# Performance work log

Measured on AMD Instinct MI355X. Metric: run time of the kernel, lower is better.

The kernel has to match this reference:

```python
import jax, jax.numpy as jnp
import numpy as np
import math

D_MODEL = 1024
EXPAND = 2
D_INNER = D_MODEL * EXPAND          # 2048
D_STATE = 16
NHEADS = 8
NGROUPS = 1
D_CONV = 4
HEADDIM = D_INNER // NHEADS         # 256
CONV_DIM = D_INNER + 2 * NGROUPS * D_STATE   # x, B, C go through the causal conv
D_IN_PROJ = 2 * D_INNER + 2 * NGROUPS * D_STATE + NHEADS  # z, xBC, dt
CHUNK = 64
BATCH = 4
SEQLEN = 4096


def setup_inputs() -> dict:
    key = jax.random.key(0)
    ks = jax.random.split(key, 6)
    rng = np.random.default_rng(0)
    u = jax.random.normal(ks[0], (BATCH, SEQLEN, D_MODEL), dtype=jnp.float32)
    W_in = jax.random.normal(ks[1], (D_MODEL, D_IN_PROJ), dtype=jnp.float32) * 0.02
    conv_w = jax.random.normal(ks[2], (CONV_DIM, D_CONV), dtype=jnp.float32) * (1.0 / math.sqrt(D_CONV))
    conv_b = jnp.zeros((CONV_DIM,), dtype=jnp.float32)
    # dt_bias = inverse-softplus of dt sampled log-uniform in [dt_min, dt_max]
    dt = np.exp(rng.uniform(size=NHEADS) * (math.log(0.1) - math.log(0.001)) + math.log(0.001))
    dt = np.clip(dt, 1e-4, None)
    dt_bias = jnp.asarray(dt + np.log(-np.expm1(-dt)), dtype=jnp.float32)
    # A in A_init_range=(0.9, 0.999), stored as A_log with A = -exp(A_log)
    A_log = jnp.asarray(np.log(rng.uniform(0.9, 0.999, NHEADS)), dtype=jnp.float32)
    D = jnp.ones((NHEADS,), dtype=jnp.float32)
    norm_w = jnp.ones((D_INNER,), dtype=jnp.float32)
    W_out = jax.random.normal(ks[3], (D_INNER, D_MODEL), dtype=jnp.float32) * 0.02
    return {"u": u, "W_in": W_in, "conv_w": conv_w, "conv_b": conv_b,
            "dt_bias": dt_bias, "A_log": A_log, "D": D, "norm_w": norm_w, "W_out": W_out}


def _mamba2_fwd(u, W_in, conv_w, conv_b, dt_bias, A_log, D, norm_w, W_out):
    b, l, _ = u.shape
    h, p, n, g, Q = NHEADS, HEADDIM, D_STATE, NGROUPS, CHUNK
    zxbcdt = u @ W_in                                   # [b,l,2*d_inner+2gn+h]
    z = zxbcdt[..., :D_INNER]
    xBC = zxbcdt[..., D_INNER:D_INNER + CONV_DIM]
    dt = jax.nn.softplus(zxbcdt[..., D_INNER + CONV_DIM:] + dt_bias)  # [b,l,h]
    # causal depthwise conv over time (d_conv taps) + SiLU
    xp = jnp.pad(xBC, ((0, 0), (D_CONV - 1, 0), (0, 0)))
    xconv = conv_b
    for k in range(D_CONV):
        xconv = xconv + xp[:, k:k + l, :] * conv_w[:, k]
    xBC = jax.nn.silu(xconv)
    x = xBC[..., :D_INNER].reshape(b, l, h, p)
    B = xBC[..., D_INNER:D_INNER + g * n].reshape(b, l, g, n)
    C = xBC[..., D_INNER + g * n:].reshape(b, l, g, n)
    Bh = jnp.repeat(B, h // g, axis=2)                  # [b,l,h,n]
    Ch = jnp.repeat(C, h // g, axis=2)
    A = -jnp.exp(A_log)                                 # [h]
    # ---- chunked (SSD) selective scan ----
    nc = l // Q
    xc = x.reshape(b, nc, Q, h, p)
    dtc = dt.reshape(b, nc, Q, h)
    Bc = Bh.reshape(b, nc, Q, h, n)
    Cc = Ch.reshape(b, nc, Q, h, n)
    a = dtc * A                                         # [b,nc,Q,h]
    cs = jnp.cumsum(a, axis=2).transpose(0, 1, 3, 2)    # [b,nc,h,Q]
    mask = jnp.tril(jnp.ones((Q, Q), dtype=bool))
    L = jnp.where(mask, jnp.exp(cs[..., :, None] - cs[..., None, :]), 0.0)  # [b,nc,h,Q,Q]
    xdt = xc * dtc[..., None]                           # x scaled by dt
    Y_diag = jnp.einsum('bcqhn,bcshn,bchqs,bcshp->bcqhp', Cc, Bc, L, xdt)
    decay_states = jnp.exp(cs[..., -1:] - cs)           # [b,nc,h,Q]
    states = jnp.einsum('bcqhn,bchq,bcqhp->bchpn', Bc, decay_states, xdt)  # per-chunk state
    chunk_decay = jnp.exp(cs[..., -1])                  # [b,nc,h]
    def step(carry, inp):
        st, dec = inp
        new = dec[..., None, None] * carry + st
        return new, carry
    init = jnp.zeros((b, h, p, n), dtype=u.dtype)
    _, prev = jax.lax.scan(step, init, (states.transpose(1, 0, 2, 3, 4), chunk_decay.transpose(1, 0, 2)))
    prev = prev.transpose(1, 0, 2, 3, 4)                # state entering each chunk [b,nc,h,p,n]
    Y_off = jnp.einsum('bcqhn,bchpn,bchq->bcqhp', Cc, prev, jnp.exp(cs))
    y = (Y_diag + Y_off).reshape(b, l, h, p) + D[:, None] * x
    y = y.reshape(b, l, D_INNER)
    # gated RMSNorm then out projection
    y = y * jax.nn.silu(z)
    y = y * jax.lax.rsqrt(jnp.mean(y * y, axis=-1, keepdims=True) + 1e-5) * norm_w
    return y @ W_out


def reference(u, W_in, conv_w, conv_b, dt_bias, A_log, D, norm_w, W_out):
    return _mamba2_fwd(u, W_in, conv_w, conv_b, dt_bias, A_log, D, norm_w, W_out)
```

## Files before the change

### kernel.cpp

```cpp
#include <hip/hip_runtime.h>
#include <cstddef>
#include <cstdint>

constexpr int DM = 1024;
constexpr int DI = 2048;
constexpr int DS = 16;
constexpr int NH = 8;
constexpr int CD = 2080;
constexpr int DP = 4136;
constexpr int DPT = 4352;
constexpr int Q  = 64;
constexpr int B_ = 4;
constexpr int L_ = 4096;
constexpr int NCH = 64;
constexpr int HP = 256;
constexpr int NR = B_ * L_;

constexpr size_t AL(size_t x) { return (x + 255) & ~(size_t)255; }
constexpr size_t OFFB_ZX = 0;
constexpr size_t OFFB_BC = AL(OFFB_ZX + (size_t)NR * DP * 2);
constexpr size_t OFFB_DT = AL(OFFB_BC + (size_t)NR * 32 * 4);
constexpr size_t OFFB_CS = AL(OFFB_DT + (size_t)NR * NH * 4);
constexpr size_t OFFB_ST = AL(OFFB_CS + (size_t)B_ * NCH * NH * Q * 4);
constexpr size_t OFFB_Y  = AL(OFFB_ST + (size_t)B_ * NCH * NH * HP * DS * 4);
constexpr size_t OFFB_WO = AL(OFFB_Y + (size_t)NR * DI * 2);

__device__ __forceinline__ float silu_f(float x) { return x / (1.f + expf(-x)); }
__device__ __forceinline__ float bf2f(unsigned short v) {
  unsigned int u = ((unsigned int)v) << 16;
  return __builtin_bit_cast(float, u);
}
__device__ __forceinline__ unsigned short f2bf(float f) {
  unsigned int u = __builtin_bit_cast(unsigned int, f);
  u += 0x7FFFu + ((u >> 16) & 1u);
  return (unsigned short)(u >> 16);
}

typedef __attribute__((ext_vector_type(8))) short bf16x8;
typedef __attribute__((ext_vector_type(4))) float f32x4;

__device__ __forceinline__ void bar() {
  asm volatile("" ::: "memory");
  __builtin_amdgcn_s_barrier();
  asm volatile("" ::: "memory");
}

template<bool OUT_BF16>
__global__ __launch_bounds__(512, 2)
void gemm256(const unsigned short* __restrict__ A, const unsigned short* __restrict__ Bt,
             void* __restrict__ Cout, int M, int N, int K, int ldc) {
  __shared__ __align__(16) unsigned short lds[2][2][2][256 * 32];
  const int t = threadIdx.x;
  const int w = t >> 6, l = t & 63;
  const int quad = l >> 4, lan = l & 15;
  const int wm = w >> 2, wn = w & 3;
  const int ncol = gridDim.x;
  const int id = blockIdx.y * ncol + blockIdx.x;
  const int xcd = id & 7, slot0 = id >> 3;
  const int rpx = gridDim.y >> 3;
  const int row_g = xcd * rpx + slot0 / ncol;
  const int col_g = slot0 - (slot0 / ncol) * ncol;
  const int row0 = row_g * 256, col0 = col_g * 256;

  const int NT = K >> 6;

  auto stage = [&](int tt, int kk, int mat) {
    const int ss = (tt < NT) ? tt : 0;
    const unsigned short* G = mat ? Bt : A;
    const int b0 = mat ? col0 : row0;
    unsigned short* lb = lds[tt & 1][kk][mat];
    const int k0 = (ss << 6) + (kk << 5);
    #pragma unroll
    for (int i = 0; i < 2; ++i) {
      const int f = i * 512 + t;
      const int pair = f >> 3, sp = f & 7;
      const int sl = sp ^ (pair & 7);
      const int r = pair * 2 + (sl >> 2);
      const int c16 = sl & 3;
      const unsigned short* gp = G + (size_t)(b0 + r) * K + k0 + (c16 << 3);
      __builtin_amdgcn_global_load_lds(
          (const __attribute__((address_space(1))) void*)gp,
          (__attribute__((address_space(3))) void*)(lb + (size_t)f * 8), 16, 0, 0);
    }
  };

  auto frag = [&](const unsigned short* base, int r, int q) -> bf16x8 {
    const int pair = r >> 1;
    const int sp = (((r & 1) << 2) | q) ^ (pair & 7);
    return *(const bf16x8*)&base[pair * 64 + sp * 8];
  };

  f32x4 acc[2][4][4];
  #pragma unroll
  for (int rq = 0; rq < 2; ++rq)
    #pragma unroll
    for (int mi = 0; mi < 4; ++mi)
      #pragma unroll
      for (int ni = 0; ni < 4; ++ni)
        acc[rq][mi][ni] = (f32x4)(0.0f);

  stage(0, 0, 0); stage(0, 0, 1);
  stage(0, 1, 0); stage(0, 1, 1);
  asm volatile("s_waitcnt vmcnt(4)" ::: "memory");
  bar();

  for (int tt = 0; tt < NT; ++tt) {
    const int cur = tt & 1;
    bf16x8 bf[4];
    #pragma unroll
    for (int p = 0; p < 4; ++p) {
      const int kk = p >> 1, rq = p & 1;
      const unsigned short* As = lds[cur][kk][0];
      const unsigned short* Bs = lds[cur][kk][1];
      bf16x8 af[4];
      #pragma unroll
      for (int mi = 0; mi < 4; ++mi)
        af[mi] = frag(As, wm * 128 + rq * 64 + mi * 16 + lan, quad);
      if (rq == 0) {
        #pragma unroll
        for (int ni = 0; ni < 4; ++ni)
          bf[ni] = frag(Bs, wn * 64 + ni * 16 + lan, quad);
      }
      stage(tt + 1, kk, rq);
      if (rq == 1)
        asm volatile("s_waitcnt vmcnt(4)" ::: "memory");
      bar();
      __builtin_amdgcn_s_setprio(1);
      #pragma unroll
      for (int mi = 0; mi < 4; ++mi)
        #pragma unroll
        for (int ni = 0; ni < 4; ++ni)
          acc[rq][mi][ni] = __builtin_amdgcn_mfma_f32_16x16x32_bf16(af[mi], bf[ni], acc[rq][mi][ni], 0, 0, 0);
      __builtin_amdgcn_s_setprio(0);
      bar();
    }
  }
  asm volatile("s_waitcnt vmcnt(0)" ::: "memory");

  #pragma unroll
  for (int rq = 0; rq < 2; ++rq)
    #pragma unroll
    for (int mi = 0; mi < 4; ++mi) {
      const size_t rb = row0 + wm * 128 + rq * 64 + mi * 16 + quad * 4;
      #pragma unroll
      for (int ni = 0; ni < 4; ++ni) {
        const int colb = col0 + wn * 64 + ni * 16 + lan;
        if (colb < N) {
          if constexpr (OUT_BF16) {
            unsigned short* C = (unsigned short*)Cout;
            #pragma unroll
            for (int r = 0; r < 4; ++r)
              C[(rb + r) * (size_t)ldc + colb] = f2bf(acc[rq][mi][ni][r]);
          } else {
            float* C = (float*)Cout;
            #pragma unroll
            for (int r = 0; r < 4; ++r)
              C[(rb + r) * (size_t)ldc + colb] = acc[rq][mi][ni][r];
          }
        }
      }
    }
}

__global__ __launch_bounds__(256)
void cvt_bf16(const float* __restrict__ src, unsigned short* __restrict__ dst, size_t n4) {
  const size_t i = ((size_t)blockIdx.x * 256 + threadIdx.x) * 4;
  if (i < n4 * 4) {
    float4 v = *(const float4*)(src + i);
    ushort4 o;
    o.x = f2bf(v.x); o.y = f2bf(v.y); o.z = f2bf(v.z); o.w = f2bf(v.w);
    *(ushort4*)(dst + i) = o;
  }
}

__global__ __launch_bounds__(256)
void transpose_cvt(const float* __restrict__ src, unsigned short* __restrict__ dst,
                   int R, int C, int Cvalid) {
  __shared__ float T[64][65];
  const int t = threadIdx.x;
  const int n0 = blockIdx.x * 64, k0 = blockIdx.y * 64;
  #pragma unroll
  for (int i = 0; i < 4; ++i) {
    int f = t + i * 256;
    int r = f >> 4, c4 = (f & 15) << 2;
    int n = n0 + c4;
    float4 v = make_float4(0.f, 0.f, 0.f, 0.f);
    if (n + 3 < Cvalid) {
      v = *(const float4*)(src + (size_t)(k0 + r) * C + n);
    } else {
      if (n + 0 < Cvalid) v.x = src[(size_t)(k0 + r) * C + n + 0];
      if (n + 1 < Cvalid) v.y = src[(size_t)(k0 + r) * C + n + 1];
      if (n + 2 < Cvalid) v.z = src[(size_t)(k0 + r) * C + n + 2];
      if (n + 3 < Cvalid) v.w = src[(size_t)(k0 + r) * C + n + 3];
    }
    T[r][c4 + 0] = v.x; T[r][c4 + 1] = v.y; T[r][c4 + 2] = v.z; T[r][c4 + 3] = v.w;
  }
  __syncthreads();
  #pragma unroll
  for (int i = 0; i < 4; ++i) {
    int f = t + i * 256;
    int c = f >> 4, r4 = (f & 15) << 2;
    ushort4 o;
    o.x = f2bf(T[r4 + 0][c]); o.y = f2bf(T[r4 + 1][c]);
    o.z = f2bf(T[r4 + 2][c]); o.w = f2bf(T[r4 + 3][c]);
    *(ushort4*)(dst + (size_t)(n0 + c) * R + k0 + r4) = o;
  }
}

__global__ __launch_bounds__(256)
void convbc_kernel(const unsigned short* __restrict__ zx, const float* __restrict__ cw,
                   const float* __restrict__ cb, float* __restrict__ bc) {
  const int idx = blockIdx.x * 256 + threadIdx.x;
  const int j = idx & 31;
  const int row = idx >> 5;
  const int l = row & (L_ - 1);
  const int cc = DI + j;
  float a = cb[cc];
  #pragma unroll
  for (int k = 0; k < 4; ++k) {
    int ll = l - 3 + k;
    if (ll >= 0)
      a += bf2f(zx[(size_t)(row - 3 + k) * DP + (DI + DI + j)]) * cw[cc * 4 + k];
  }
  bc[(size_t)row * 32 + j] = silu_f(a);
}

__global__ __launch_bounds__(256)
void dt_kernel(const unsigned short* __restrict__ zx, const float* __restrict__ dt_bias,
               float* __restrict__ dt) {
  const int i = blockIdx.x * 256 + threadIdx.x;
  const int h = i & 7;
  const size_t row = (size_t)(i >> 3);
  float x = bf2f(zx[row * DP + (DI + CD) + h]) + dt_bias[h];
  dt[i] = (x > 20.f) ? x : log1pf(expf(x));
}

__global__ __launch_bounds__(256)
void chunk_kernel(const unsigned short* __restrict__ zx, const float* __restrict__ bc,
                  const float* __restrict__ dt, const float* __restrict__ A_log,
                  const float* __restrict__ cw, const float* __restrict__ cb,
                  const float* __restrict__ Dp, float* __restrict__ cs_out,
                  float* __restrict__ states, unsigned short* __restrict__ yb) {
  const int c = blockIdx.x, h = blockIdx.y, b = blockIdx.z;
  const int t = threadIdx.x;
  const int w = t >> 6, l = t & 63;
  const int quad = l >> 4, lan = l & 15;
  __shared__ float dtS[Q], csS[Q], ddS[Q];
  __shared__ float BsS[Q][DS + 1];
  __shared__ __align__(16) unsigned short Msd[Q][Q + 8];
  __shared__ __align__(16) unsigned short BdT[DS][Q + 8];
  __shared__ __align__(16) char regionA[Q * (Q + 8) * 2];
  __shared__ __align__(16) char regionB[Q * DS * 4 + Q * (Q + 8) * 2];
  float (*CsS)[DS]                 = (float(*)[DS])regionA;
  unsigned short (*xsT)[Q + 8]     = (unsigned short(*)[Q + 8])regionA;
  unsigned short (*rawS)[Q]        = (unsigned short(*)[Q])regionB;
  float (*stS)[DS]                 = (float(*)[DS])regionB;
  unsigned short (*ytS)[Q + 8]     = (unsigned short(*)[Q + 8])(regionB + Q * DS * 4);
  const size_t rowb = (size_t)b * L_ + (size_t)c * Q;

  if (t < Q) {
    float dtv = dt[(rowb + t) * NH + h];
    dtS[t] = dtv;
    float s = dtv * (-expf(A_log[h]));
    #pragma unroll
    for (int off = 1; off < 64; off <<= 1) {
      float n = __shfl_up(s, off, 64);
      if (t >= off) s += n;
    }
    csS[t] = s;
    float slast = __shfl(s, 63, 64);
    ddS[t] = expf(slast - s) * dtv;
    cs_out[(((size_t)b * NCH + c) * NH + h) * Q + t] = s;
  }
  for (int i = t; i < Q * DS; i += 256) {
    int q = i >> 4, n = i & 15;
    BsS[q][n] = bc[(rowb + q) * 32 + n];
    CsS[q][n] = bc[(rowb + q) * 32 + 16 + n];
  }
  __syncthreads();
  for (int i = t; i < DS * Q; i += 256) {
    int n = i & 15, q = i >> 4;
    BdT[n][q] = f2bf(BsS[q][n] * ddS[q]);
  }
  const float Dh = Dp[h];
  for (int i = t; i < Q * Q; i += 256) {
    int q = i >> 6, s = i & 63;
    float v = 0.f;
    if (s <= q) {
      float d = 0.f;
      #pragma unroll
      for (int n = 0; n < DS; ++n) d += CsS[q][n] * BsS[s][n];
      v = expf(csS[q] - csS[s]) * d * dtS[s];
      if (s == q) v += Dh;
    }
    Msd[q][s] = f2bf(v);
  }

  const int pch = l;
  uint4 r0 = make_uint4(0, 0, 0, 0), r1 = make_uint4(0, 0, 0, 0), r2 = make_uint4(0, 0, 0, 0);
  {
    const int col0 = DI + h * HP;
    const unsigned short* gb = zx + ((size_t)b * L_ + (c * Q - 3)) * DP + col0;
    if (c > 0 || t >= 24) r0 = *(const uint4*)(gb + (size_t)(t >> 3) * DP + (t & 7) * 8);
    r1 = *(const uint4*)(gb + (size_t)((t + 256) >> 3) * DP + (t & 7) * 8);
    if (t < 24) r2 = *(const uint4*)(gb + (size_t)((t + 512) >> 3) * DP + (t & 7) * 8);
  }

  for (int pt = 0; pt < 4; ++pt) {
    uint4* rw = (uint4*)rawS;
    rw[t] = r0; rw[t + 256] = r1;
    if (t < 24) rw[t + 512] = r2;
    __syncthreads();
    {
      const int cc = h * HP + pt * Q + pch;
      const float w0 = cw[cc * 4 + 0], w1 = cw[cc * 4 + 1];
      const float w2 = cw[cc * 4 + 2], w3 = cw[cc * 4 + 3];
      const float bias = cb[cc];
      const int q0 = w * 16;
      unsigned short ob[16];
      #pragma unroll
      for (int i2 = 0; i2 < 16; ++i2) {
        int q = q0 + i2;
        float a = bias + bf2f(rawS[q][pch]) * w0 + bf2f(rawS[q + 1][pch]) * w1
                       + bf2f(rawS[q + 2][pch]) * w2 + bf2f(rawS[q + 3][pch]) * w3;
        ob[i2] = f2bf(silu_f(a));
      }
      *(uint4*)&xsT[pch][q0 + 0] = *(uint4*)&ob[0];
      *(uint4*)&xsT[pch][q0 + 8] = *(uint4*)&ob[8];
    }
    if (pt < 3) {
      const int col0n = DI + h * HP + (pt + 1) * Q;
      const unsigned short* gb = zx + ((size_t)b * L_ + (c * Q - 3)) * DP + col0n;
      r0 = make_uint4(0, 0, 0, 0); r2 = make_uint4(0, 0, 0, 0);
      if (c > 0 || t >= 24) r0 = *(const uint4*)(gb + (size_t)(t >> 3) * DP + (t & 7) * 8);
      r1 = *(const uint4*)(gb + (size_t)((t + 256) >> 3) * DP + (t & 7) * 8);
      if (t < 24) r2 = *(const uint4*)(gb + (size_t)((t + 512) >> 3) * DP + (t & 7) * 8);
    }
    __syncthreads();
    bf16x8 xfrag[2];
    #pragma unroll
    for (int ks = 0; ks < 2; ++ks)
      xfrag[ks] = *(const bf16x8*)&xsT[w * 16 + lan][quad * 8 + ks * 32];
    {
      f32x4 sacc = (f32x4)(0.0f);
      #pragma unroll
      for (int ks = 0; ks < 2; ++ks) {
        bf16x8 bfr = *(const bf16x8*)&BdT[lan][quad * 8 + ks * 32];
        sacc = __builtin_amdgcn_mfma_f32_16x16x32_bf16(xfrag[ks], bfr, sacc, 0, 0, 0);
      }
      #pragma unroll
      for (int r = 0; r < 4; ++r)
        stS[w * 16 + quad * 4 + r][lan] = sacc[r];
    }
    {
      #pragma unroll
      for (int mi = 0; mi < 4; ++mi) {
        f32x4 yac = (f32x4)(0.0f);
        #pragma unroll
        for (int ks = 0; ks < 2; ++ks) {
          bf16x8 am = *(const bf16x8*)&Msd[mi * 16 + lan][quad * 8 + ks * 32];
          yac = __builtin_amdgcn_mfma_f32_16x16x32_bf16(am, xfrag[ks], yac, 0, 0, 0);
        }
        #pragma unroll
        for (int r = 0; r < 4; ++r)
          ytS[mi * 16 + quad * 4 + r][w * 16 + lan] = f2bf(yac[r]);
      }
    }
    __syncthreads();
    {
      const size_t stbase = ((((size_t)b * NCH + c) * NH + h) * HP + (size_t)pt * Q) * DS;
      ((float4*)(states + stbase))[t] = ((const float4*)&stS[0][0])[t];
    }
    {
      const int colbase = h * HP + pt * Q;
      #pragma unroll
      for (int pass = 0; pass < 2; ++pass) {
        int q = pass * 32 + (t >> 3), p8 = (t & 7) * 8;
        *(uint4*)(yb + (rowb + q) * (size_t)DI + colbase + p8) = *(const uint4*)&ytS[q][p8];
      }
    }
    __syncthreads();
  }
}

__global__ __launch_bounds__(256)
void scan_kernel(float* __restrict__ states, const float* __restrict__ cs) {
  const int pn = blockIdx.x * 256 + threadIdx.x;
  const int h = blockIdx.y, b = blockIdx.z;
  const size_t cstride = (size_t)NH * HP * DS;
  const size_t base = ((size_t)b * NCH * NH + h) * (size_t)(HP * DS) + pn;
  float carry = 0.f;
  for (int c = 0; c < NCH; ++c) {
    float dec = expf(cs[(((size_t)b * NCH + c) * NH + h) * Q + (Q - 1)]);
    float st = states[base + (size_t)c * cstride];
    states[base + (size_t)c * cstride] = carry;
    carry = dec * carry + st;
  }
}

__global__ __launch_bounds__(256)
void yoff_kernel(const float* __restrict__ bc, const float* __restrict__ cs,
                 const float* __restrict__ prev, unsigned short* __restrict__ yb) {
  const int c = blockIdx.x, h = blockIdx.y, b = blockIdx.z;
  const int t = threadIdx.x;
  __shared__ __align__(16) float CsS[Q][DS];
  __shared__ float ecs[Q];
  const size_t rowb = (size_t)b * L_ + (size_t)c * Q;
  const size_t pb = (((size_t)b * NCH + c) * NH + h) * (size_t)(HP * DS);
  for (int i = t; i < Q * DS; i += 256) {
    int q = i >> 4, n = i & 15;
    CsS[q][n] = bc[(rowb + q) * 32 + 16 + n];
  }
  if (t < Q) ecs[t] = expf(cs[(((size_t)b * NCH + c) * NH + h) * Q + t]);
  float pv[16];
  #pragma unroll
  for (int k = 0; k < 4; ++k)
    *(float4*)&pv[k * 4] = *(const float4*)(prev + pb + (size_t)t * DS + k * 4);
  __syncthreads();
  for (int q = 0; q < Q; ++q) {
    float acc = 0.f;
    #pragma unroll
    for (int n = 0; n < DS; ++n) acc += CsS[q][n] * pv[n];
    const size_t idx = (rowb + q) * DI + h * HP + t;
    yb[idx] = f2bf(bf2f(yb[idx]) + ecs[q] * acc);
  }
}

__global__ __launch_bounds__(256)
void gatenorm_kernel(const unsigned short* __restrict__ zx, const float* __restrict__ norm_w,
                     unsigned short* __restrict__ yb) {
  const size_t row = blockIdx.x;
  const int t = threadIdx.x;
  const unsigned short* zrow = zx + row * DP;
  unsigned short* yrow = yb + row * DI;
  const int d0 = t * 8;
  uint4 yv = *(const uint4*)(yrow + d0);
  uint4 zv = *(const uint4*)(zrow + d0);
  const unsigned short* ys = (const unsigned short*)&yv;
  const unsigned short* zs = (const unsigned short*)&zv;
  float v[8];
  float ss = 0.f;
  #pragma unroll
  for (int j = 0; j < 8; ++j) {
    float val = bf2f(ys[j]) * silu_f(bf2f(zs[j]));
    v[j] = val;
    ss += val * val;
  }
  #pragma unroll
  for (int off = 32; off > 0; off >>= 1) ss += __shfl_down(ss, off);
  __shared__ float red[4];
  if ((t & 63) == 0) red[t >> 6] = ss;
  __syncthreads();
  float tot = red[0] + red[1] + red[2] + red[3];
  float scale = rsqrtf(tot / (float)DI + 1e-5f);
  ushort4 o[2];
  unsigned short* op = (unsigned short*)o;
  #pragma unroll
  for (int j = 0; j < 8; ++j) op[j] = f2bf(v[j] * scale * norm_w[d0 + j]);
  *(uint4*)(yrow + d0) = *(uint4*)o;
}

extern "C" void kernel_launch(void* const* d_in, const int* in_sizes, int n_in,
                              void* d_out, int out_size, void* d_ws, size_t ws_size,
                              hipStream_t stream) {
  const float* u       = (const float*)d_in[0];
  const float* W_in    = (const float*)d_in[1];
  const float* conv_w  = (const float*)d_in[2];
  const float* conv_b  = (const float*)d_in[3];
  const float* dt_bias = (const float*)d_in[4];
  const float* A_log   = (const float*)d_in[5];
  const float* Dp      = (const float*)d_in[6];
  const float* norm_w  = (const float*)d_in[7];
  const float* W_out   = (const float*)d_in[8];
  float* out = (float*)d_out;
  char* w = (char*)d_ws;

  unsigned short* zx  = (unsigned short*)(w + OFFB_ZX);
  float* bcb          = (float*)(w + OFFB_BC);
  float* dtb          = (float*)(w + OFFB_DT);
  float* csb          = (float*)(w + OFFB_CS);
  float* stb          = (float*)(w + OFFB_ST);
  unsigned short* yb  = (unsigned short*)(w + OFFB_Y);
  unsigned short* ub  = (unsigned short*)(w + OFFB_ST);
  unsigned short* wib = (unsigned short*)(w + OFFB_Y);
  unsigned short* wob = (unsigned short*)(w + OFFB_WO);

  cvt_bf16<<<(NR * DM / 4 + 255) / 256, 256, 0, stream>>>(u, ub, (size_t)NR * DM / 4);
  transpose_cvt<<<dim3(DPT / 64, DM / 64), 256, 0, stream>>>(W_in, wib, DM, DP, DP);
  transpose_cvt<<<dim3(DM / 64, DI / 64), 256, 0, stream>>>(W_out, wob, DI, DM, DM);
  gemm256<true><<<dim3(DPT / 256, NR / 256), 512, 0, stream>>>(
      ub, wib, zx, NR, DP, DM, DP);
  convbc_kernel<<<(NR * 32) / 256, 256, 0, stream>>>(zx, conv_w, conv_b, bcb);
  dt_kernel<<<(NR * NH) / 256, 256, 0, stream>>>(zx, dt_bias, dtb);
  chunk_kernel<<<dim3(NCH, NH, B_), 256, 0, stream>>>(zx, bcb, dtb, A_log, conv_w,
                                                      conv_b, Dp, csb, stb, yb);
  scan_kernel<<<dim3((HP * DS) / 256, NH, B_), 256, 0, stream>>>(stb, csb);
  yoff_kernel<<<dim3(NCH, NH, B_), 256, 0, stream>>>(bcb, csb, stb, yb);
  gatenorm_kernel<<<NR, 256, 0, stream>>>(zx, norm_w, yb);
  gemm256<false><<<dim3(DM / 256, NR / 256), 512, 0, stream>>>(
      yb, wob, out, NR, DM, DI, DM);
}
```

Baseline: 532.8 us.

## Replace direct global-to-LDS loads with register-staged prefetch and one barrier per tile

The GEMM main loop stops using global_load_lds DMA with four barriers per K-tile. Instead it loads the next tile's halves into registers, stores them to the other LDS buffer after each half's MFMAs, and syncs once per iteration. This is meant to cut barrier overhead and let the compiler overlap global loads with compute. In exchange it uses more VGPRs for staging, adds VMEM-to-register waits before the LDS stores, and may lower occupancy.

```diff
diff --git a/kernel.cpp b/kernel.cpp
--- a/kernel.cpp
+++ b/kernel.cpp
@@ -38,12 +38,6 @@
 
 typedef __attribute__((ext_vector_type(8))) short bf16x8;
 typedef __attribute__((ext_vector_type(4))) float f32x4;
-
-__device__ __forceinline__ void bar() {
-  asm volatile("" ::: "memory");
-  __builtin_amdgcn_s_barrier();
-  asm volatile("" ::: "memory");
-}
 
 template<bool OUT_BF16>
 __global__ __launch_bounds__(512, 2)
@@ -64,24 +58,34 @@
 
   const int NT = K >> 6;
 
-  auto stage = [&](int tt, int kk, int mat) {
-    const int ss = (tt < NT) ? tt : 0;
+  auto gaddr = [&](int tt, int kk, int mat, int i) -> const unsigned short* {
     const unsigned short* G = mat ? Bt : A;
     const int b0 = mat ? col0 : row0;
-    unsigned short* lb = lds[tt & 1][kk][mat];
-    const int k0 = (ss << 6) + (kk << 5);
-    #pragma unroll
-    for (int i = 0; i < 2; ++i) {
-      const int f = i * 512 + t;
-      const int pair = f >> 3, sp = f & 7;
-      const int sl = sp ^ (pair & 7);
-      const int r = pair * 2 + (sl >> 2);
-      const int c16 = sl & 3;
-      const unsigned short* gp = G + (size_t)(b0 + r) * K + k0 + (c16 << 3);
-      __builtin_amdgcn_global_load_lds(
-          (const __attribute__((address_space(1))) void*)gp,
-          (__attribute__((address_space(3))) void*)(lb + (size_t)f * 8), 16, 0, 0);
-    }
+    const int k0 = (tt << 6) + (kk << 5);
+    const int f = i * 512 + t;
+    const int pair = f >> 3, sp = f & 7;
+    const int sl = sp ^ (pair & 7);
+    const int r = pair * 2 + (sl >> 2);
+    const int c16 = sl & 3;
+    return G + (size_t)(b0 + r) * K + k0 + (c16 << 3);
+  };
+
+  uint4 st[2][2];
+  auto issueH = [&](int tt, int kk) {
+    #pragma unroll
+    for (int mat = 0; mat < 2; ++mat)
+      #pragma unroll
+      for (int i = 0; i < 2; ++i)
+        st[mat][i] = *(const uint4*)gaddr(tt, kk, mat, i);
+  };
+  auto commitH = [&](int buf, int kk) {
+    #pragma unroll
+    for (int mat = 0; mat < 2; ++mat)
+      #pragma unroll
+      for (int i = 0; i < 2; ++i) {
+        const int f = i * 512 + t;
+        *(uint4*)&lds[buf][kk][mat][(size_t)f * 8] = st[mat][i];
+      }
   };
 
   auto frag = [&](const unsigned short* base, int r, int q) -> bf16x8 {
@@ -99,19 +103,21 @@
       for (int ni = 0; ni < 4; ++ni)
         acc[rq][mi][ni] = (f32x4)(0.0f);
 
-  stage(0, 0, 0); stage(0, 0, 1);
-  stage(0, 1, 0); stage(0, 1, 1);
-  asm volatile("s_waitcnt vmcnt(4)" ::: "memory");
-  bar();
+  issueH(0, 0); commitH(0, 0);
+  issueH(0, 1); commitH(0, 1);
+  asm volatile("s_waitcnt lgkmcnt(0)" ::: "memory");
+  asm volatile("s_barrier" ::: "memory");
 
   for (int tt = 0; tt < NT; ++tt) {
     const int cur = tt & 1;
+    const int nxt = cur ^ 1;
+    const bool pf = (tt + 1 < NT);
+    if (pf) issueH(tt + 1, 0);
     bf16x8 bf[4];
     #pragma unroll
-    for (int p = 0; p < 4; ++p) {
-      const int kk = p >> 1, rq = p & 1;
-      const unsigned short* As = lds[cur][kk][0];
-      const unsigned short* Bs = lds[cur][kk][1];
+    for (int rq = 0; rq < 2; ++rq) {
+      const unsigned short* As = lds[cur][0][0];
+      const unsigned short* Bs = lds[cur][0][1];
       bf16x8 af[4];
       #pragma unroll
       for (int mi = 0; mi < 4; ++mi)
@@ -121,10 +127,6 @@
         for (int ni = 0; ni < 4; ++ni)
           bf[ni] = frag(Bs, wn * 64 + ni * 16 + lan, quad);
       }
-      stage(tt + 1, kk, rq);
-      if (rq == 1)
-        asm volatile("s_waitcnt vmcnt(4)" ::: "memory");
-      bar();
       __builtin_amdgcn_s_setprio(1);
       #pragma unroll
       for (int mi = 0; mi < 4; ++mi)
@@ -132,10 +134,33 @@
         for (int ni = 0; ni < 4; ++ni)
           acc[rq][mi][ni] = __builtin_amdgcn_mfma_f32_16x16x32_bf16(af[mi], bf[ni], acc[rq][mi][ni], 0, 0, 0);
       __builtin_amdgcn_s_setprio(0);
-      bar();
-    }
-  }
-  asm volatile("s_waitcnt vmcnt(0)" ::: "memory");
+    }
+    if (pf) { commitH(nxt, 0); issueH(tt + 1, 1); }
+    #pragma unroll
+    for (int rq = 0; rq < 2; ++rq) {
+      const unsigned short* As = lds[cur][1][0];
+      const unsigned short* Bs = lds[cur][1][1];
+      bf16x8 af[4];
+      #pragma unroll
+      for (int mi = 0; mi < 4; ++mi)
+        af[mi] = frag(As, wm * 128 + rq * 64 + mi * 16 + lan, quad);
+      if (rq == 0) {
+        #pragma unroll
+        for (int ni = 0; ni < 4; ++ni)
+          bf[ni] = frag(Bs, wn * 64 + ni * 16 + lan, quad);
+      }
+      __builtin_amdgcn_s_setprio(1);
+      #pragma unroll
+      for (int mi = 0; mi < 4; ++mi)
+        #pragma unroll
+        for (int ni = 0; ni < 4; ++ni)
+          acc[rq][mi][ni] = __builtin_amdgcn_mfma_f32_16x16x32_bf16(af[mi], bf[ni], acc[rq][mi][ni], 0, 0, 0);
+      __builtin_amdgcn_s_setprio(0);
+    }
+    if (pf) commitH(nxt, 1);
+    asm volatile("s_waitcnt lgkmcnt(0)" ::: "memory");
+    asm volatile("s_barrier" ::: "memory");
+  }
 
   #pragma unroll
   for (int rq = 0; rq < 2; ++rq)
```

Result: slower. 650.3 us (+22.0%).

## Software-pipeline LDS fragment loads ahead of MFMA in GEMM main loop

Applied to the files above, without the earlier changes.

Restructures the GEMM inner loop so that the LDS fragment reads for the next sub-tile are issued before the MFMA block of the current sub-tile, using double-buffered register fragments (af0/af1, bf0/bf1). It removes one of the two barriers per sub-step and adds sched_barrier hints to keep the ordering. The goal is to hide LDS read latency behind matrix-core work and cut barrier stalls. In exchange it raises register pressure at 2 blocks per CU, and the LDS reuse is only protected by the remaining barriers.

```diff
diff --git a/kernel.cpp b/kernel.cpp
--- a/kernel.cpp
+++ b/kernel.cpp
@@ -38,12 +38,6 @@
 
 typedef __attribute__((ext_vector_type(8))) short bf16x8;
 typedef __attribute__((ext_vector_type(4))) float f32x4;
-
-__device__ __forceinline__ void bar() {
-  asm volatile("" ::: "memory");
-  __builtin_amdgcn_s_barrier();
-  asm volatile("" ::: "memory");
-}
 
 template<bool OUT_BF16>
 __global__ __launch_bounds__(512, 2)
@@ -99,41 +93,80 @@
       for (int ni = 0; ni < 4; ++ni)
         acc[rq][mi][ni] = (f32x4)(0.0f);
 
+  bf16x8 af0[4], af1[4], bf0[4], bf1[4];
+
   stage(0, 0, 0); stage(0, 0, 1);
   stage(0, 1, 0); stage(0, 1, 1);
   asm volatile("s_waitcnt vmcnt(4)" ::: "memory");
-  bar();
+  __builtin_amdgcn_s_barrier();
+  __builtin_amdgcn_sched_barrier(0);
+  #pragma unroll
+  for (int mi = 0; mi < 4; ++mi)
+    af0[mi] = frag(lds[0][0][0], wm * 128 + mi * 16 + lan, quad);
+  #pragma unroll
+  for (int ni = 0; ni < 4; ++ni)
+    bf0[ni] = frag(lds[0][0][1], wn * 64 + ni * 16 + lan, quad);
 
   for (int tt = 0; tt < NT; ++tt) {
-    const int cur = tt & 1;
-    bf16x8 bf[4];
-    #pragma unroll
-    for (int p = 0; p < 4; ++p) {
-      const int kk = p >> 1, rq = p & 1;
-      const unsigned short* As = lds[cur][kk][0];
-      const unsigned short* Bs = lds[cur][kk][1];
-      bf16x8 af[4];
-      #pragma unroll
-      for (int mi = 0; mi < 4; ++mi)
-        af[mi] = frag(As, wm * 128 + rq * 64 + mi * 16 + lan, quad);
-      if (rq == 0) {
-        #pragma unroll
-        for (int ni = 0; ni < 4; ++ni)
-          bf[ni] = frag(Bs, wn * 64 + ni * 16 + lan, quad);
-      }
-      stage(tt + 1, kk, rq);
-      if (rq == 1)
-        asm volatile("s_waitcnt vmcnt(4)" ::: "memory");
-      bar();
-      __builtin_amdgcn_s_setprio(1);
-      #pragma unroll
-      for (int mi = 0; mi < 4; ++mi)
-        #pragma unroll
-        for (int ni = 0; ni < 4; ++ni)
-          acc[rq][mi][ni] = __builtin_amdgcn_mfma_f32_16x16x32_bf16(af[mi], bf[ni], acc[rq][mi][ni], 0, 0, 0);
-      __builtin_amdgcn_s_setprio(0);
-      bar();
-    }
+    const int cur = tt & 1, nb = cur ^ 1;
+    stage(tt + 1, 0, 0);
+    __builtin_amdgcn_s_barrier();
+    #pragma unroll
+    for (int mi = 0; mi < 4; ++mi)
+      af1[mi] = frag(lds[cur][0][0], wm * 128 + 64 + mi * 16 + lan, quad);
+    __builtin_amdgcn_s_setprio(1);
+    #pragma unroll
+    for (int mi = 0; mi < 4; ++mi)
+      #pragma unroll
+      for (int ni = 0; ni < 4; ++ni)
+        acc[0][mi][ni] = __builtin_amdgcn_mfma_f32_16x16x32_bf16(af0[mi], bf0[ni], acc[0][mi][ni], 0, 0, 0);
+    __builtin_amdgcn_s_setprio(0);
+    stage(tt + 1, 0, 1);
+    asm volatile("s_waitcnt vmcnt(4)" ::: "memory");
+    __builtin_amdgcn_s_barrier();
+    __builtin_amdgcn_sched_barrier(0);
+    #pragma unroll
+    for (int mi = 0; mi < 4; ++mi)
+      af0[mi] = frag(lds[cur][1][0], wm * 128 + mi * 16 + lan, quad);
+    #pragma unroll
+    for (int ni = 0; ni < 4; ++ni)
+      bf1[ni] = frag(lds[cur][1][1], wn * 64 + ni * 16 + lan, quad);
+    __builtin_amdgcn_s_setprio(1);
+    #pragma unroll
+    for (int mi = 0; mi < 4; ++mi)
+      #pragma unroll
+      for (int ni = 0; ni < 4; ++ni)
+        acc[1][mi][ni] = __builtin_amdgcn_mfma_f32_16x16x32_bf16(af1[mi], bf0[ni], acc[1][mi][ni], 0, 0, 0);
+    __builtin_amdgcn_s_setprio(0);
+    stage(tt + 1, 1, 0);
+    __builtin_amdgcn_s_barrier();
+    #pragma unroll
+    for (int mi = 0; mi < 4; ++mi)
+      af1[mi] = frag(lds[cur][1][0], wm * 128 + 64 + mi * 16 + lan, quad);
+    __builtin_amdgcn_s_setprio(1);
+    #pragma unroll
+    for (int mi = 0; mi < 4; ++mi)
+      #pragma unroll
+      for (int ni = 0; ni < 4; ++ni)
+        acc[0][mi][ni] = __builtin_amdgcn_mfma_f32_16x16x32_bf16(af0[mi], bf1[ni], acc[0][mi][ni], 0, 0, 0);
+    __builtin_amdgcn_s_setprio(0);
+    stage(tt + 1, 1, 1);
+    asm volatile("s_waitcnt vmcnt(4)" ::: "memory");
+    __builtin_amdgcn_s_barrier();
+    __builtin_amdgcn_sched_barrier(0);
+    #pragma unroll
+    for (int mi = 0; mi < 4; ++mi)
+      af0[mi] = frag(lds[nb][0][0], wm * 128 + mi * 16 + lan, quad);
+    #pragma unroll
+    for (int ni = 0; ni < 4; ++ni)
+      bf0[ni] = frag(lds[nb][0][1], wn * 64 + ni * 16 + lan, quad);
+    __builtin_amdgcn_s_setprio(1);
+    #pragma unroll
+    for (int mi = 0; mi < 4; ++mi)
+      #pragma unroll
+      for (int ni = 0; ni < 4; ++ni)
+        acc[1][mi][ni] = __builtin_amdgcn_mfma_f32_16x16x32_bf16(af1[mi], bf1[ni], acc[1][mi][ni], 0, 0, 0);
+    __builtin_amdgcn_s_setprio(0);
   }
   asm volatile("s_waitcnt vmcnt(0)" ::: "memory");
 
```

New measurement: 536.0 us. About the same (+0.6%).
